# Kernel tuning notes

Hardware: AMD Instinct MI355X
Metric: run time of the kernel (lower is better)

Reference implementation:

```python
import jax, jax.numpy as jnp
import numpy as np

B, EEG_D, FMRI_D, BD, H, NC = 131072, 128, 64, 128, 4, 2
HD = BD // H  # head dim = 32
EPS = 1e-5

def layernorm(x, g, b):
    m = jnp.mean(x, axis=-1, keepdims=True)
    v = jnp.var(x, axis=-1, keepdims=True)
    return (x - m) * jax.lax.rsqrt(v + EPS) * g + b

def setup_inputs() -> dict:
    key = jax.random.key(0)
    ks = jax.random.split(key, 24)
    r = lambda i, shape, s=0.05: jax.random.normal(ks[i], shape, dtype=jnp.float32) * s
    return {
        'eeg_feats': jax.random.normal(ks[0], (B, EEG_D), dtype=jnp.float32),
        'fmri_feats': jax.random.normal(ks[1], (B, FMRI_D), dtype=jnp.float32),
        # projections (weights stored [in, out])
        'We': r(2, (EEG_D, BD)), 'be': jnp.zeros((BD,)),
        'ge': jnp.ones((BD,)), 'bge': jnp.zeros((BD,)),
        'Wf': r(3, (FMRI_D, BD)), 'bf': jnp.zeros((BD,)),
        'gf': jnp.ones((BD,)), 'bgf': jnp.zeros((BD,)),
        # multihead attention
        'Wq': r(4, (BD, BD)), 'bq': jnp.zeros((BD,)),
        'Wk': r(5, (BD, BD)), 'bk': jnp.zeros((BD,)),
        'Wv': r(6, (BD, BD)), 'bv': jnp.zeros((BD,)),
        'Wo': r(7, (BD, BD)), 'bo': jnp.zeros((BD,)),
        # learned fusion
        'fusion_logits': jnp.zeros((2,)),
        'temperature': jnp.ones(()),
        # classifier
        'Wc1': r(8, (BD, BD // 2)), 'bc1': jnp.zeros((BD // 2,)),
        'gc': jnp.ones((BD // 2,)), 'bgc': jnp.zeros((BD // 2,)),
        'Wc2': r(9, (BD // 2, NC)), 'bc2': jnp.zeros((NC,)),
    }

def reference(eeg_feats, fmri_feats, We, be, ge, bge, Wf, bf, gf, bgf,
              Wq, bq, Wk, bk, Wv, bv, Wo, bo, fusion_logits, temperature,
              Wc1, bc1, gc, bgc, Wc2, bc2):
    # modality projections: Linear + LN + GELU (dropout off at eval)
    eeg_p = jax.nn.gelu(layernorm(eeg_feats @ We + be, ge, bge), approximate=False)
    fmri_p = jax.nn.gelu(layernorm(fmri_feats @ Wf + bf, gf, bgf), approximate=False)

    # cross-attention: query = eeg_p (1 token), kv = [eeg_p, fmri_p] (2 tokens)
    seq = jnp.stack([eeg_p, fmri_p], axis=1)                 # [B, 2, BD]
    q = (eeg_p @ Wq + bq).reshape(B, H, HD)                  # [B, H, HD]
    k = (seq @ Wk + bk).reshape(B, 2, H, HD)
    v = (seq @ Wv + bv).reshape(B, 2, H, HD)
    scores = jnp.einsum('bhd,bkhd->bhk', q, k) / jnp.sqrt(jnp.float32(HD))
    attn = jax.nn.softmax(scores, axis=-1)                   # [B, H, 2]
    ctx = jnp.einsum('bhk,bkhd->bhd', attn, v).reshape(B, BD)
    eeg_enh = ctx @ Wo + bo                                  # [B, BD]

    # learned temperature-scaled fusion over [eeg_enhanced, fmri_proj]
    w = jax.nn.softmax(fusion_logits / temperature, axis=0)
    fused = w[0] * eeg_enh + w[1] * fmri_p                   # [B, BD]

    # classifier: Linear + LN + ReLU + Linear
    h = jax.nn.relu(layernorm(fused @ Wc1 + bc1, gc, bgc))
    logits = h @ Wc2 + bc2                                   # [B, NC]
    return logits
```

## Files before the change

kernel.cpp:

```cpp
#include <hip/hip_runtime.h>
#include <math.h>

#define EPS 1e-5f
#define SCALE 0.17677669529663687f

#define OFF_We  0
#define OFF_Wf  16384
#define OFF_Wq  24576
#define OFF_Wk  40960
#define OFF_Wv  57344
#define OFF_Wo  73728
#define OFF_Wc1 90112
#define PACK_TOTAL 98304

#define CHUNK 4096

#define BOFF(r, c) ((((r) << 7) + (c)) ^ (((r) & 7) << 3))

typedef __bf16 bf16x8 __attribute__((ext_vector_type(8)));
typedef float f32x4 __attribute__((ext_vector_type(4)));
typedef unsigned short ushort_t;
typedef unsigned short ushortx4 __attribute__((ext_vector_type(4)));

__device__ __forceinline__ ushort_t f2bf(float x) {
    return __builtin_bit_cast(ushort_t, (__bf16)x);
}
__device__ __forceinline__ float bf2f(ushort_t v) {
    unsigned u = ((unsigned)v) << 16;
    return __builtin_bit_cast(float, u);
}

__device__ __forceinline__ ushort_t f2bf_sw(float x) {
    unsigned u = __builtin_bit_cast(unsigned, x);
    u = (u + 0x7fffu + ((u >> 16) & 1u)) >> 16;
    return (ushort_t)u;
}

#define DPPADD(x, ctrl) \
    ((x) + __builtin_bit_cast(float, __builtin_amdgcn_update_dpp( \
        __builtin_bit_cast(int, (x)), __builtin_bit_cast(int, (x)), (ctrl), 0xF, 0xF, false)))

__device__ __forceinline__ float rowsum16(float x) {
    x = DPPADD(x, 0x121);
    x = DPPADD(x, 0x122);
    x = DPPADD(x, 0x124);
    x = DPPADD(x, 0x128);
    return x;
}

__device__ __forceinline__ float gelu_fast(float x) {
    float x2 = x * x;
    float t = fmaf(-0.10294313843f, x2, -2.30220842f);
#if __has_builtin(__builtin_amdgcn_exp2f)
    float e = __builtin_amdgcn_exp2f(x * t);
#else
    float e = __expf(x * t * 0.6931471806f);
#endif
    return x * __builtin_amdgcn_rcpf(1.0f + e);
}

__global__ __launch_bounds__(256) void pack_all(
    const float* __restrict__ We, const float* __restrict__ Wf,
    const float* __restrict__ Wq, const float* __restrict__ Wk,
    const float* __restrict__ Wv, const float* __restrict__ Wo,
    const float* __restrict__ Wc1, ushort_t* __restrict__ ws)
{
    int o = blockIdx.x * 256 + threadIdx.x;
    if (o >= PACK_TOTAL) return;
    const float* W; int K, N, base;
    if (o < OFF_Wf)        { W = We;  K = 128; N = 128; base = OFF_We; }
    else if (o < OFF_Wq)   { W = Wf;  K = 64;  N = 128; base = OFF_Wf; }
    else if (o < OFF_Wk)   { W = Wq;  K = 128; N = 128; base = OFF_Wq; }
    else if (o < OFF_Wv)   { W = Wk;  K = 128; N = 128; base = OFF_Wk; }
    else if (o < OFF_Wo)   { W = Wv;  K = 128; N = 128; base = OFF_Wv; }
    else if (o < OFF_Wc1)  { W = Wo;  K = 128; N = 128; base = OFF_Wo; }
    else                   { W = Wc1; K = 128; N = 64;  base = OFF_Wc1; }
    int e = o - base;
    int j = e & 7, l = (e >> 3) & 63, rest = e >> 9;
    int KS = K >> 5;
    int s = rest % KS, t = rest / KS;
    int k = s * 32 + ((l >> 4) << 3) + j;
    int n = (t << 4) + (l & 15);
    ws[o] = f2bf_sw(W[k * N + n]);
}

template<int KS>
__device__ __forceinline__ void load_af(bf16x8 af[KS], const ushort_t* A, int lane)
{
    const int quad = lane >> 4, l16 = lane & 15;
    #pragma unroll
    for (int ks = 0; ks < KS; ++ks)
        af[ks] = *(const bf16x8*)(A + BOFF(l16, ks * 32 + quad * 8));
}

template<int KS, int NT>
__device__ __forceinline__ void mma_c(const bf16x8 af[KS], const ushort_t* sW,
                                      f32x4* acc, int lane)
{
    #pragma unroll
    for (int t = 0; t < NT; ++t)
        #pragma unroll
        for (int ks = 0; ks < KS; ++ks) {
            bf16x8 bb = *(const bf16x8*)(sW + ((t * KS + ks) * 64 + lane) * 8);
            acc[t] = __builtin_amdgcn_mfma_f32_16x16x32_bf16(af[ks], bb, acc[t], 0, 0, 0);
        }
}

__global__ __launch_bounds__(256, 3) void fusion_stage(
    const float* __restrict__ eeg, const float* __restrict__ fmri,
    const float* __restrict__ be, const float* __restrict__ ge, const float* __restrict__ bge,
    const float* __restrict__ bfb, const float* __restrict__ gf, const float* __restrict__ bgf,
    const float* __restrict__ bq, const float* __restrict__ bk, const float* __restrict__ bv,
    const float* __restrict__ bo,
    const float* __restrict__ fusion_logits, const float* __restrict__ temperature,
    const float* __restrict__ bc1, const float* __restrict__ gc, const float* __restrict__ bgc,
    const float* __restrict__ Wc2, const float* __restrict__ bc2,
    const ushort_t* __restrict__ ws, float* __restrict__ out)
{
    __shared__ __align__(16) ushort_t sW[CHUNK];
    __shared__ __align__(16) ushort_t B1[4][16 * 128];
    __shared__ __align__(16) ushort_t B2[4][16 * 128];

    const int tid = threadIdx.x;
    const int wave = tid >> 6, lane = tid & 63;
    const int quad = lane >> 4, l16 = lane & 15;
    const int rowbase = blockIdx.x * 64 + wave * 16;
    ushort_t* b1 = B1[wave];
    ushort_t* b2 = B2[wave];

    auto stageW = [&](int offU) {
        __syncthreads();
        const char* g = (const char*)(ws + offU) + tid * 16;
        char* l = (char*)sW + tid * 16;
        __builtin_amdgcn_global_load_lds(
            (const __attribute__((address_space(1))) void*)g,
            (__attribute__((address_space(3))) void*)l, 16, 0, 0);
        __builtin_amdgcn_global_load_lds(
            (const __attribute__((address_space(1))) void*)(g + 4096),
            (__attribute__((address_space(3))) void*)(l + 4096), 16, 0, 0);
        __syncthreads();
    };

    {
        const float4* src = (const float4*)(eeg + (size_t)rowbase * 128);
        #pragma unroll
        for (int i = 0; i < 8; ++i) {
            int idx = i * 64 + lane;
            float4 v = src[idx];
            int r = idx >> 5, k4 = (idx & 31) * 4;
            *(ushortx4*)&b1[BOFF(r, k4)] =
                (ushortx4){f2bf(v.x), f2bf(v.y), f2bf(v.z), f2bf(v.w)};
        }
        const float4* srcf = (const float4*)(fmri + (size_t)rowbase * 64);
        #pragma unroll
        for (int i = 0; i < 4; ++i) {
            int idx = i * 64 + lane;
            float4 v = srcf[idx];
            int r = idx >> 4, k4 = (idx & 15) * 4;
            *(ushortx4*)&b2[BOFF(r, k4)] =
                (ushortx4){f2bf(v.x), f2bf(v.y), f2bf(v.z), f2bf(v.w)};
        }
    }

    float meanS[4], rstdS[4];

    {
        bf16x8 afR[4]; load_af<4>(afR, b1, lane);
        f32x4 acc[8];
        #pragma unroll
        for (int nt = 0; nt < 8; ++nt) {
            float b = be[nt * 16 + l16];
            acc[nt] = (f32x4){b, b, b, b};
        }
        #pragma unroll
        for (int c = 0; c < 4; ++c) {
            stageW(OFF_We + c * CHUNK);
            mma_c<4, 2>(afR, sW, acc + c * 2, lane);
        }
        #pragma unroll
        for (int r = 0; r < 4; ++r) {
            float s = 0.f, ss = 0.f;
            #pragma unroll
            for (int nt = 0; nt < 8; ++nt) { float x = acc[nt][r]; s += x; ss = fmaf(x, x, ss); }
            s = rowsum16(s); ss = rowsum16(ss);
            float m = s * (1.f / 128.f);
            meanS[r] = m;
            rstdS[r] = rsqrtf(ss * (1.f / 128.f) - m * m + EPS);
        }
        #pragma unroll
        for (int nt = 0; nt < 8; ++nt) {
            float g = ge[nt * 16 + l16], bb = bge[nt * 16 + l16];
            #pragma unroll
            for (int r = 0; r < 4; ++r) {
                float x = (acc[nt][r] - meanS[r]) * rstdS[r] * g + bb;
                b1[BOFF(quad * 4 + r, nt * 16 + l16)] = f2bf(gelu_fast(x));
            }
        }
    }

    f32x4 fpv[8];
    {
        bf16x8 afR[2]; load_af<2>(afR, b2, lane);
        f32x4 acc[8];
        #pragma unroll
        for (int nt = 0; nt < 8; ++nt) {
            float b = bfb[nt * 16 + l16];
            acc[nt] = (f32x4){b, b, b, b};
        }
        stageW(OFF_Wf);          mma_c<2, 4>(afR, sW, acc + 0, lane);
        stageW(OFF_Wf + CHUNK);  mma_c<2, 4>(afR, sW, acc + 4, lane);
        #pragma unroll
        for (int r = 0; r < 4; ++r) {
            float s = 0.f, ss = 0.f;
            #pragma unroll
            for (int nt = 0; nt < 8; ++nt) { float x = acc[nt][r]; s += x; ss = fmaf(x, x, ss); }
            s = rowsum16(s); ss = rowsum16(ss);
            float m = s * (1.f / 128.f);
            meanS[r] = m;
            rstdS[r] = rsqrtf(ss * (1.f / 128.f) - m * m + EPS);
        }
        #pragma unroll
        for (int nt = 0; nt < 8; ++nt) {
            float g = gf[nt * 16 + l16], bb = bgf[nt * 16 + l16];
            #pragma unroll
            for (int r = 0; r < 4; ++r) {
                float x = (acc[nt][r] - meanS[r]) * rstdS[r] * g + bb;
                float gv = gelu_fast(x);
                fpv[nt][r] = gv;
                b2[BOFF(quad * 4 + r, nt * 16 + l16)] = f2bf(gv);
            }
        }
    }

    bf16x8 afE[4]; load_af<4>(afE, b1, lane);
    bf16x8 afF[4]; load_af<4>(afF, b2, lane);

    f32x4 q[8];
    {
        #pragma unroll
        for (int nt = 0; nt < 8; ++nt) {
            float b = bq[nt * 16 + l16];
            q[nt] = (f32x4){b, b, b, b};
        }
        #pragma unroll
        for (int c = 0; c < 4; ++c) {
            stageW(OFF_Wq + c * CHUNK);
            mma_c<4, 2>(afE, sW, q + c * 2, lane);
        }
    }

    float a0v[4][4];
    {
        float pd[4][4];
        #pragma unroll
        for (int h = 0; h < 4; ++h)
            #pragma unroll
            for (int r = 0; r < 4; ++r) pd[h][r] = 0.f;
        #pragma unroll
        for (int c = 0; c < 4; ++c) {
            stageW(OFF_Wk + c * CHUNK);
            #pragma unroll
            for (int tl = 0; tl < 2; ++tl) {
                int nt = c * 2 + tl;
                f32x4 e = {0.f, 0.f, 0.f, 0.f}, f = {0.f, 0.f, 0.f, 0.f};
                #pragma unroll
                for (int ks = 0; ks < 4; ++ks) {
                    bf16x8 bb = *(const bf16x8*)(sW + ((tl * 4 + ks) * 64 + lane) * 8);
                    e = __builtin_amdgcn_mfma_f32_16x16x32_bf16(afE[ks], bb, e, 0, 0, 0);
                    f = __builtin_amdgcn_mfma_f32_16x16x32_bf16(afF[ks], bb, f, 0, 0, 0);
                }
                int h = nt >> 1;
                #pragma unroll
                for (int r = 0; r < 4; ++r)
                    pd[h][r] = fmaf(q[nt][r], e[r] - f[r], pd[h][r]);
            }
        }
        #pragma unroll
        for (int h = 0; h < 4; ++h)
            #pragma unroll
            for (int r = 0; r < 4; ++r) {
                float d = rowsum16(pd[h][r]) * SCALE;
                a0v[h][r] = __builtin_amdgcn_rcpf(1.0f + __expf(-d));
            }
    }

    #pragma unroll
    for (int c = 0; c < 4; ++c) {
        stageW(OFF_Wv + c * CHUNK);
        #pragma unroll
        for (int tl = 0; tl < 2; ++tl) {
            int nt = c * 2 + tl;
            float b = bv[nt * 16 + l16];
            f32x4 e = {b, b, b, b}, f = {b, b, b, b};
            #pragma unroll
            for (int ks = 0; ks < 4; ++ks) {
                bf16x8 bb = *(const bf16x8*)(sW + ((tl * 4 + ks) * 64 + lane) * 8);
                e = __builtin_amdgcn_mfma_f32_16x16x32_bf16(afE[ks], bb, e, 0, 0, 0);
                f = __builtin_amdgcn_mfma_f32_16x16x32_bf16(afF[ks], bb, f, 0, 0, 0);
            }
            int h = nt >> 1;
            #pragma unroll
            for (int r = 0; r < 4; ++r) {
                float c0 = fmaf(a0v[h][r], e[r] - f[r], f[r]);
                b1[BOFF(quad * 4 + r, nt * 16 + l16)] = f2bf(c0);
            }
        }
    }

    {
        bf16x8 afC[4]; load_af<4>(afC, b1, lane);
        f32x4 acc[8];
        #pragma unroll
        for (int nt = 0; nt < 8; ++nt) {
            float b = bo[nt * 16 + l16];
            acc[nt] = (f32x4){b, b, b, b};
        }
        #pragma unroll
        for (int c = 0; c < 4; ++c) {
            stageW(OFF_Wo + c * CHUNK);
            mma_c<4, 2>(afC, sW, acc + c * 2, lane);
        }
        float t = temperature[0];
        float dl = (fusion_logits[0] - fusion_logits[1]) / t;
        float w0 = __builtin_amdgcn_rcpf(1.0f + __expf(-dl));
        float w1 = 1.0f - w0;
        #pragma unroll
        for (int nt = 0; nt < 8; ++nt)
            #pragma unroll
            for (int r = 0; r < 4; ++r)
                b1[BOFF(quad * 4 + r, nt * 16 + l16)] = f2bf(w0 * acc[nt][r] + w1 * fpv[nt][r]);
    }

    {
        bf16x8 afU[4]; load_af<4>(afU, b1, lane);
        f32x4 accH[4];
        #pragma unroll
        for (int nt = 0; nt < 4; ++nt) {
            float b = bc1[nt * 16 + l16];
            accH[nt] = (f32x4){b, b, b, b};
        }
        stageW(OFF_Wc1);          mma_c<4, 2>(afU, sW, accH + 0, lane);
        stageW(OFF_Wc1 + CHUNK);  mma_c<4, 2>(afU, sW, accH + 2, lane);
        #pragma unroll
        for (int r = 0; r < 4; ++r) {
            float s = 0.f, ss = 0.f;
            #pragma unroll
            for (int nt = 0; nt < 4; ++nt) { float x = accH[nt][r]; s += x; ss = fmaf(x, x, ss); }
            s = rowsum16(s); ss = rowsum16(ss);
            float m = s * (1.f / 64.f);
            meanS[r] = m;
            rstdS[r] = rsqrtf(ss * (1.f / 64.f) - m * m + EPS);
        }
        float hv[4][4];
        #pragma unroll
        for (int nt = 0; nt < 4; ++nt) {
            float g = gc[nt * 16 + l16], bb = bgc[nt * 16 + l16];
            #pragma unroll
            for (int r = 0; r < 4; ++r) {
                float x = (accH[nt][r] - meanS[r]) * rstdS[r] * g + bb;
                hv[nt][r] = fmaxf(x, 0.0f);
            }
        }
        float w2v[4][2];
        #pragma unroll
        for (int nt = 0; nt < 4; ++nt) {
            float2 w = *(const float2*)&Wc2[(nt * 16 + l16) * 2];
            w2v[nt][0] = w.x; w2v[nt][1] = w.y;
        }
        float o0c = bc2[0], o1c = bc2[1];
        #pragma unroll
        for (int r = 0; r < 4; ++r) {
            float p0 = 0.f, p1 = 0.f;
            #pragma unroll
            for (int nt = 0; nt < 4; ++nt) {
                p0 = fmaf(hv[nt][r], w2v[nt][0], p0);
                p1 = fmaf(hv[nt][r], w2v[nt][1], p1);
            }
            p0 = rowsum16(p0); p1 = rowsum16(p1);
            if (l16 == 0) {
                int row = rowbase + quad * 4 + r;
                float2 o; o.x = p0 + o0c; o.y = p1 + o1c;
                *(float2*)&out[row * 2] = o;
            }
        }
    }
}

extern "C" void kernel_launch(void* const* d_in, const int* in_sizes, int n_in,
                              void* d_out, int out_size, void* d_ws, size_t ws_size,
                              hipStream_t stream) {
    const float* eeg  = (const float*)d_in[0];
    const float* fmri = (const float*)d_in[1];
    const float* We   = (const float*)d_in[2];
    const float* be   = (const float*)d_in[3];
    const float* ge   = (const float*)d_in[4];
    const float* bge  = (const float*)d_in[5];
    const float* Wf   = (const float*)d_in[6];
    const float* bf   = (const float*)d_in[7];
    const float* gf   = (const float*)d_in[8];
    const float* bgf  = (const float*)d_in[9];
    const float* Wq   = (const float*)d_in[10];
    const float* bq   = (const float*)d_in[11];
    const float* Wk   = (const float*)d_in[12];
    const float* bk   = (const float*)d_in[13];
    const float* Wv   = (const float*)d_in[14];
    const float* bv   = (const float*)d_in[15];
    const float* Wo   = (const float*)d_in[16];
    const float* bo   = (const float*)d_in[17];
    const float* fl   = (const float*)d_in[18];
    const float* temp = (const float*)d_in[19];
    const float* Wc1  = (const float*)d_in[20];
    const float* bc1  = (const float*)d_in[21];
    const float* gc   = (const float*)d_in[22];
    const float* bgc  = (const float*)d_in[23];
    const float* Wc2  = (const float*)d_in[24];
    const float* bc2  = (const float*)d_in[25];
    float* out = (float*)d_out;
    ushort_t* ws = (ushort_t*)d_ws;

    hipLaunchKernelGGL(pack_all, dim3((PACK_TOTAL + 255) / 256), dim3(256), 0, stream,
                       We, Wf, Wq, Wk, Wv, Wo, Wc1, ws);

    int B = in_sizes[0] / 128;
    int grid = B / 64;
    hipLaunchKernelGGL(fusion_stage, dim3(grid), dim3(256), 0, stream,
                       eeg, fmri, be, ge, bge, bf, gf, bgf,
                       bq, bk, bv, bo, fl, temp, bc1, gc, bgc, Wc2, bc2,
                       ws, out);
}
```

Baseline: 235.3 us.

## Double-buffer weight chunk staging and prefetch next chunk during MFMA compute

Weight staging changes from a single LDS buffer with two barriers per chunk to two ping-pong buffers. Each step issues an asynchronous global-to-LDS load of the next chunk right after one barrier, so weight fetches overlap the current chunk's MFMAs. The second per-wave activation buffer is removed and its data reuses the first buffer in sequence, which cuts LDS usage. The cost is more LDS for weights, and correctness now depends on the barrier waiting for the outstanding async loads.

```diff
diff --git a/kernel.cpp b/kernel.cpp
--- a/kernel.cpp
+++ b/kernel.cpp
@@ -14,6 +14,7 @@
 #define PACK_TOTAL 98304
 
 #define CHUNK 4096
+#define NCHUNK 24
 
 #define BOFF(r, c) ((((r) << 7) + (c)) ^ (((r) & 7) << 3))
 
@@ -94,14 +95,14 @@
 }
 
 template<int KS, int NT>
-__device__ __forceinline__ void mma_c(const bf16x8 af[KS], const ushort_t* sW,
+__device__ __forceinline__ void mma_c(const bf16x8 af[KS], const ushort_t* sWb,
                                       f32x4* acc, int lane)
 {
     #pragma unroll
     for (int t = 0; t < NT; ++t)
         #pragma unroll
         for (int ks = 0; ks < KS; ++ks) {
-            bf16x8 bb = *(const bf16x8*)(sW + ((t * KS + ks) * 64 + lane) * 8);
+            bf16x8 bb = *(const bf16x8*)(sWb + ((t * KS + ks) * 64 + lane) * 8);
             acc[t] = __builtin_amdgcn_mfma_f32_16x16x32_bf16(af[ks], bb, acc[t], 0, 0, 0);
         }
 }
@@ -117,29 +118,36 @@
     const float* __restrict__ Wc2, const float* __restrict__ bc2,
     const ushort_t* __restrict__ ws, float* __restrict__ out)
 {
-    __shared__ __align__(16) ushort_t sW[CHUNK];
+    __shared__ __align__(16) ushort_t sW[2][CHUNK];
     __shared__ __align__(16) ushort_t B1[4][16 * 128];
-    __shared__ __align__(16) ushort_t B2[4][16 * 128];
 
     const int tid = threadIdx.x;
     const int wave = tid >> 6, lane = tid & 63;
     const int quad = lane >> 4, l16 = lane & 15;
     const int rowbase = blockIdx.x * 64 + wave * 16;
     ushort_t* b1 = B1[wave];
-    ushort_t* b2 = B2[wave];
-
-    auto stageW = [&](int offU) {
-        __syncthreads();
-        const char* g = (const char*)(ws + offU) + tid * 16;
-        char* l = (char*)sW + tid * 16;
+
+    auto prefetch = [&](int c) {
+        const char* g = (const char*)(ws + c * CHUNK) + tid * 16;
+        char* l = (char*)(sW[c & 1]) + tid * 16;
         __builtin_amdgcn_global_load_lds(
             (const __attribute__((address_space(1))) void*)g,
             (__attribute__((address_space(3))) void*)l, 16, 0, 0);
         __builtin_amdgcn_global_load_lds(
             (const __attribute__((address_space(1))) void*)(g + 4096),
             (__attribute__((address_space(3))) void*)(l + 4096), 16, 0, 0);
+    };
+
+    int ck = 0;
+    auto step = [&]() -> const ushort_t* {
         __syncthreads();
+        if (ck + 1 < NCHUNK) prefetch(ck + 1);
+        const ushort_t* p = sW[ck & 1];
+        ++ck;
+        return p;
     };
+
+    prefetch(0);
 
     {
         const float4* src = (const float4*)(eeg + (size_t)rowbase * 128);
@@ -151,32 +159,35 @@
             *(ushortx4*)&b1[BOFF(r, k4)] =
                 (ushortx4){f2bf(v.x), f2bf(v.y), f2bf(v.z), f2bf(v.w)};
         }
+    }
+    bf16x8 afR[4]; load_af<4>(afR, b1, lane);
+
+    {
         const float4* srcf = (const float4*)(fmri + (size_t)rowbase * 64);
         #pragma unroll
         for (int i = 0; i < 4; ++i) {
             int idx = i * 64 + lane;
             float4 v = srcf[idx];
             int r = idx >> 4, k4 = (idx & 15) * 4;
-            *(ushortx4*)&b2[BOFF(r, k4)] =
+            *(ushortx4*)&b1[BOFF(r, k4)] =
                 (ushortx4){f2bf(v.x), f2bf(v.y), f2bf(v.z), f2bf(v.w)};
         }
     }
+    bf16x8 afRf[2]; load_af<2>(afRf, b1, lane);
 
     float meanS[4], rstdS[4];
 
     {
-        bf16x8 afR[4]; load_af<4>(afR, b1, lane);
         f32x4 acc[8];
         #pragma unroll
         for (int nt = 0; nt < 8; ++nt) {
             float b = be[nt * 16 + l16];
             acc[nt] = (f32x4){b, b, b, b};
         }
-        #pragma unroll
-        for (int c = 0; c < 4; ++c) {
-            stageW(OFF_We + c * CHUNK);
-            mma_c<4, 2>(afR, sW, acc + c * 2, lane);
-        }
+        mma_c<4, 2>(afR, step(), acc + 0, lane);
+        mma_c<4, 2>(afR, step(), acc + 2, lane);
+        mma_c<4, 2>(afR, step(), acc + 4, lane);
+        mma_c<4, 2>(afR, step(), acc + 6, lane);
         #pragma unroll
         for (int r = 0; r < 4; ++r) {
             float s = 0.f, ss = 0.f;
@@ -200,15 +211,14 @@
 
     f32x4 fpv[8];
     {
-        bf16x8 afR[2]; load_af<2>(afR, b2, lane);
         f32x4 acc[8];
         #pragma unroll
         for (int nt = 0; nt < 8; ++nt) {
             float b = bfb[nt * 16 + l16];
             acc[nt] = (f32x4){b, b, b, b};
         }
-        stageW(OFF_Wf);          mma_c<2, 4>(afR, sW, acc + 0, lane);
-        stageW(OFF_Wf + CHUNK);  mma_c<2, 4>(afR, sW, acc + 4, lane);
+        mma_c<2, 4>(afRf, step(), acc + 0, lane);
+        mma_c<2, 4>(afRf, step(), acc + 4, lane);
         #pragma unroll
         for (int r = 0; r < 4; ++r) {
             float s = 0.f, ss = 0.f;
@@ -225,15 +235,18 @@
             #pragma unroll
             for (int r = 0; r < 4; ++r) {
                 float x = (acc[nt][r] - meanS[r]) * rstdS[r] * g + bb;
-                float gv = gelu_fast(x);
-                fpv[nt][r] = gv;
-                b2[BOFF(quad * 4 + r, nt * 16 + l16)] = f2bf(gv);
+                fpv[nt][r] = gelu_fast(x);
             }
         }
     }
 
     bf16x8 afE[4]; load_af<4>(afE, b1, lane);
-    bf16x8 afF[4]; load_af<4>(afF, b2, lane);
+    #pragma unroll
+    for (int nt = 0; nt < 8; ++nt)
+        #pragma unroll
+        for (int r = 0; r < 4; ++r)
+            b1[BOFF(quad * 4 + r, nt * 16 + l16)] = f2bf(fpv[nt][r]);
+    bf16x8 afF[4]; load_af<4>(afF, b1, lane);
 
     f32x4 q[8];
     {
@@ -242,30 +255,29 @@
             float b = bq[nt * 16 + l16];
             q[nt] = (f32x4){b, b, b, b};
         }
+        mma_c<4, 2>(afE, step(), q + 0, lane);
+        mma_c<4, 2>(afE, step(), q + 2, lane);
+        mma_c<4, 2>(afE, step(), q + 4, lane);
+        mma_c<4, 2>(afE, step(), q + 6, lane);
+    }
+
+    float a0v[4][4];
+    {
+        float pd[4][4];
+        #pragma unroll
+        for (int h = 0; h < 4; ++h)
+            #pragma unroll
+            for (int r = 0; r < 4; ++r) pd[h][r] = 0.f;
         #pragma unroll
         for (int c = 0; c < 4; ++c) {
-            stageW(OFF_Wq + c * CHUNK);
-            mma_c<4, 2>(afE, sW, q + c * 2, lane);
-        }
-    }
-
-    float a0v[4][4];
-    {
-        float pd[4][4];
-        #pragma unroll
-        for (int h = 0; h < 4; ++h)
-            #pragma unroll
-            for (int r = 0; r < 4; ++r) pd[h][r] = 0.f;
-        #pragma unroll
-        for (int c = 0; c < 4; ++c) {
-            stageW(OFF_Wk + c * CHUNK);
+            const ushort_t* p = step();
             #pragma unroll
             for (int tl = 0; tl < 2; ++tl) {
                 int nt = c * 2 + tl;
                 f32x4 e = {0.f, 0.f, 0.f, 0.f}, f = {0.f, 0.f, 0.f, 0.f};
                 #pragma unroll
                 for (int ks = 0; ks < 4; ++ks) {
-                    bf16x8 bb = *(const bf16x8*)(sW + ((tl * 4 + ks) * 64 + lane) * 8);
+                    bf16x8 bb = *(const bf16x8*)(p + ((tl * 4 + ks) * 64 + lane) * 8);
                     e = __builtin_amdgcn_mfma_f32_16x16x32_bf16(afE[ks], bb, e, 0, 0, 0);
                     f = __builtin_amdgcn_mfma_f32_16x16x32_bf16(afF[ks], bb, f, 0, 0, 0);
                 }
@@ -286,7 +298,7 @@
 
     #pragma unroll
     for (int c = 0; c < 4; ++c) {
-        stageW(OFF_Wv + c * CHUNK);
+        const ushort_t* p = step();
         #pragma unroll
         for (int tl = 0; tl < 2; ++tl) {
             int nt = c * 2 + tl;
@@ -294,7 +306,7 @@
             f32x4 e = {b, b, b, b}, f = {b, b, b, b};
             #pragma unroll
             for (int ks = 0; ks < 4; ++ks) {
-                bf16x8 bb = *(const bf16x8*)(sW + ((tl * 4 + ks) * 64 + lane) * 8);
+                bf16x8 bb = *(const bf16x8*)(p + ((tl * 4 + ks) * 64 + lane) * 8);
                 e = __builtin_amdgcn_mfma_f32_16x16x32_bf16(afE[ks], bb, e, 0, 0, 0);
                 f = __builtin_amdgcn_mfma_f32_16x16x32_bf16(afF[ks], bb, f, 0, 0, 0);
             }
@@ -315,11 +327,10 @@
             float b = bo[nt * 16 + l16];
             acc[nt] = (f32x4){b, b, b, b};
         }
-        #pragma unroll
-        for (int c = 0; c < 4; ++c) {
-            stageW(OFF_Wo + c * CHUNK);
-            mma_c<4, 2>(afC, sW, acc + c * 2, lane);
-        }
+        mma_c<4, 2>(afC, step(), acc + 0, lane);
+        mma_c<4, 2>(afC, step(), acc + 2, lane);
+        mma_c<4, 2>(afC, step(), acc + 4, lane);
+        mma_c<4, 2>(afC, step(), acc + 6, lane);
         float t = temperature[0];
         float dl = (fusion_logits[0] - fusion_logits[1]) / t;
         float w0 = __builtin_amdgcn_rcpf(1.0f + __expf(-dl));
@@ -339,8 +350,8 @@
             float b = bc1[nt * 16 + l16];
             accH[nt] = (f32x4){b, b, b, b};
         }
-        stageW(OFF_Wc1);          mma_c<4, 2>(afU, sW, accH + 0, lane);
-        stageW(OFF_Wc1 + CHUNK);  mma_c<4, 2>(afU, sW, accH + 2, lane);
+        mma_c<4, 2>(afU, step(), accH + 0, lane);
+        mma_c<4, 2>(afU, step(), accH + 2, lane);
         #pragma unroll
         for (int r = 0; r < 4; ++r) {
             float s = 0.f, ss = 0.f;
```

After: 230.9 us. About the same (-1.9%).

## Stage weights in 32KB chunks to cut barrier count and drop second activation buffer

Applied to the files above, without the earlier changes.

Weight staging grows from 8KB to 32KB chunks, so the packed weights load in 6 stages instead of 24, each stage followed by __syncthreads. The matmuls are regrouped so each chunk covers the tail of one weight matrix and the head of the next, and the K/V projections are split across chunk boundaries. The separate B2 activation buffer is removed and B1 is reused, which reorders loads and stores. This cuts barrier and load-issue overhead, but the larger LDS footprint (about 48KB total) may reduce the number of blocks resident per CU and weaken latency hiding.

```diff
diff --git a/kernel.cpp b/kernel.cpp
--- a/kernel.cpp
+++ b/kernel.cpp
@@ -13,7 +13,8 @@
 #define OFF_Wc1 90112
 #define PACK_TOTAL 98304
 
-#define CHUNK 4096
+#define CHUNK 16384
+#define HALF  8192
 
 #define BOFF(r, c) ((((r) << 7) + (c)) ^ (((r) & 7) << 3))
 
@@ -94,14 +95,14 @@
 }
 
 template<int KS, int NT>
-__device__ __forceinline__ void mma_c(const bf16x8 af[KS], const ushort_t* sW,
+__device__ __forceinline__ void mma_c(const bf16x8 af[KS], const ushort_t* p,
                                       f32x4* acc, int lane)
 {
     #pragma unroll
     for (int t = 0; t < NT; ++t)
         #pragma unroll
         for (int ks = 0; ks < KS; ++ks) {
-            bf16x8 bb = *(const bf16x8*)(sW + ((t * KS + ks) * 64 + lane) * 8);
+            bf16x8 bb = *(const bf16x8*)(p + ((t * KS + ks) * 64 + lane) * 8);
             acc[t] = __builtin_amdgcn_mfma_f32_16x16x32_bf16(af[ks], bb, acc[t], 0, 0, 0);
         }
 }
@@ -119,25 +120,22 @@
 {
     __shared__ __align__(16) ushort_t sW[CHUNK];
     __shared__ __align__(16) ushort_t B1[4][16 * 128];
-    __shared__ __align__(16) ushort_t B2[4][16 * 128];
 
     const int tid = threadIdx.x;
     const int wave = tid >> 6, lane = tid & 63;
     const int quad = lane >> 4, l16 = lane & 15;
     const int rowbase = blockIdx.x * 64 + wave * 16;
     ushort_t* b1 = B1[wave];
-    ushort_t* b2 = B2[wave];
-
-    auto stageW = [&](int offU) {
+
+    auto stageW = [&](int c) {
         __syncthreads();
-        const char* g = (const char*)(ws + offU) + tid * 16;
+        const char* g = (const char*)(ws + c * CHUNK) + tid * 16;
         char* l = (char*)sW + tid * 16;
-        __builtin_amdgcn_global_load_lds(
-            (const __attribute__((address_space(1))) void*)g,
-            (__attribute__((address_space(3))) void*)l, 16, 0, 0);
-        __builtin_amdgcn_global_load_lds(
-            (const __attribute__((address_space(1))) void*)(g + 4096),
-            (__attribute__((address_space(3))) void*)(l + 4096), 16, 0, 0);
+        #pragma unroll
+        for (int i = 0; i < 8; ++i)
+            __builtin_amdgcn_global_load_lds(
+                (const __attribute__((address_space(1))) void*)(g + i * 4096),
+                (__attribute__((address_space(3))) void*)(l + i * 4096), 16, 0, 0);
         __syncthreads();
     };
 
@@ -151,32 +149,33 @@
             *(ushortx4*)&b1[BOFF(r, k4)] =
                 (ushortx4){f2bf(v.x), f2bf(v.y), f2bf(v.z), f2bf(v.w)};
         }
+    }
+    bf16x8 afR[4]; load_af<4>(afR, b1, lane);
+
+    {
         const float4* srcf = (const float4*)(fmri + (size_t)rowbase * 64);
         #pragma unroll
         for (int i = 0; i < 4; ++i) {
             int idx = i * 64 + lane;
             float4 v = srcf[idx];
             int r = idx >> 4, k4 = (idx & 15) * 4;
-            *(ushortx4*)&b2[BOFF(r, k4)] =
+            *(ushortx4*)&b1[BOFF(r, k4)] =
                 (ushortx4){f2bf(v.x), f2bf(v.y), f2bf(v.z), f2bf(v.w)};
         }
     }
+    bf16x8 afRf[2]; load_af<2>(afRf, b1, lane);
 
     float meanS[4], rstdS[4];
 
-    {
-        bf16x8 afR[4]; load_af<4>(afR, b1, lane);
+    stageW(0);
+    {
         f32x4 acc[8];
         #pragma unroll
         for (int nt = 0; nt < 8; ++nt) {
             float b = be[nt * 16 + l16];
             acc[nt] = (f32x4){b, b, b, b};
         }
-        #pragma unroll
-        for (int c = 0; c < 4; ++c) {
-            stageW(OFF_We + c * CHUNK);
-            mma_c<4, 2>(afR, sW, acc + c * 2, lane);
-        }
+        mma_c<4, 8>(afR, sW, acc, lane);
         #pragma unroll
         for (int r = 0; r < 4; ++r) {
             float s = 0.f, ss = 0.f;
@@ -199,16 +198,17 @@
     }
 
     f32x4 fpv[8];
-    {
-        bf16x8 afR[2]; load_af<2>(afR, b2, lane);
+    f32x4 q[8];
+    bf16x8 afE[4], afF[4];
+    stageW(1);
+    {
         f32x4 acc[8];
         #pragma unroll
         for (int nt = 0; nt < 8; ++nt) {
             float b = bfb[nt * 16 + l16];
             acc[nt] = (f32x4){b, b, b, b};
         }
-        stageW(OFF_Wf);          mma_c<2, 4>(afR, sW, acc + 0, lane);
-        stageW(OFF_Wf + CHUNK);  mma_c<2, 4>(afR, sW, acc + 4, lane);
+        mma_c<2, 8>(afRf, sW, acc, lane);
         #pragma unroll
         for (int r = 0; r < 4; ++r) {
             float s = 0.f, ss = 0.f;
@@ -225,73 +225,56 @@
             #pragma unroll
             for (int r = 0; r < 4; ++r) {
                 float x = (acc[nt][r] - meanS[r]) * rstdS[r] * g + bb;
-                float gv = gelu_fast(x);
-                fpv[nt][r] = gv;
-                b2[BOFF(quad * 4 + r, nt * 16 + l16)] = f2bf(gv);
-            }
-        }
-    }
-
-    bf16x8 afE[4]; load_af<4>(afE, b1, lane);
-    bf16x8 afF[4]; load_af<4>(afF, b2, lane);
-
-    f32x4 q[8];
-    {
+                fpv[nt][r] = gelu_fast(x);
+            }
+        }
+        load_af<4>(afE, b1, lane);
+        #pragma unroll
+        for (int nt = 0; nt < 8; ++nt)
+            #pragma unroll
+            for (int r = 0; r < 4; ++r)
+                b1[BOFF(quad * 4 + r, nt * 16 + l16)] = f2bf(fpv[nt][r]);
+        load_af<4>(afF, b1, lane);
         #pragma unroll
         for (int nt = 0; nt < 8; ++nt) {
             float b = bq[nt * 16 + l16];
             q[nt] = (f32x4){b, b, b, b};
         }
-        #pragma unroll
-        for (int c = 0; c < 4; ++c) {
-            stageW(OFF_Wq + c * CHUNK);
-            mma_c<4, 2>(afE, sW, q + c * 2, lane);
+        mma_c<4, 4>(afE, sW + HALF, q + 0, lane);
+    }
+
+    float pd[4][4];
+    #pragma unroll
+    for (int h = 0; h < 4; ++h)
+        #pragma unroll
+        for (int r = 0; r < 4; ++r) pd[h][r] = 0.f;
+    stageW(2);
+    {
+        mma_c<4, 4>(afE, sW, q + 4, lane);
+        #pragma unroll
+        for (int tl = 0; tl < 4; ++tl) {
+            int nt = tl;
+            f32x4 e = {0.f, 0.f, 0.f, 0.f}, f = {0.f, 0.f, 0.f, 0.f};
+            #pragma unroll
+            for (int ks = 0; ks < 4; ++ks) {
+                bf16x8 bb = *(const bf16x8*)(sW + HALF + ((tl * 4 + ks) * 64 + lane) * 8);
+                e = __builtin_amdgcn_mfma_f32_16x16x32_bf16(afE[ks], bb, e, 0, 0, 0);
+                f = __builtin_amdgcn_mfma_f32_16x16x32_bf16(afF[ks], bb, f, 0, 0, 0);
+            }
+            int h = nt >> 1;
+            #pragma unroll
+            for (int r = 0; r < 4; ++r)
+                pd[h][r] = fmaf(q[nt][r], e[r] - f[r], pd[h][r]);
         }
     }
 
     float a0v[4][4];
-    {
-        float pd[4][4];
-        #pragma unroll
-        for (int h = 0; h < 4; ++h)
-            #pragma unroll
-            for (int r = 0; r < 4; ++r) pd[h][r] = 0.f;
-        #pragma unroll
-        for (int c = 0; c < 4; ++c) {
-            stageW(OFF_Wk + c * CHUNK);
-            #pragma unroll
-            for (int tl = 0; tl < 2; ++tl) {
-                int nt = c * 2 + tl;
-                f32x4 e = {0.f, 0.f, 0.f, 0.f}, f = {0.f, 0.f, 0.f, 0.f};
-                #pragma unroll
-                for (int ks = 0; ks < 4; ++ks) {
-                    bf16x8 bb = *(const bf16x8*)(sW + ((tl * 4 + ks) * 64 + lane) * 8);
-                    e = __builtin_amdgcn_mfma_f32_16x16x32_bf16(afE[ks], bb, e, 0, 0, 0);
-                    f = __builtin_amdgcn_mfma_f32_16x16x32_bf16(afF[ks], bb, f, 0, 0, 0);
-                }
-                int h = nt >> 1;
-                #pragma unroll
-                for (int r = 0; r < 4; ++r)
-                    pd[h][r] = fmaf(q[nt][r], e[r] - f[r], pd[h][r]);
-            }
-        }
-        #pragma unroll
-        for (int h = 0; h < 4; ++h)
-            #pragma unroll
-            for (int r = 0; r < 4; ++r) {
-                float d = rowsum16(pd[h][r]) * SCALE;
-                a0v[h][r] = __builtin_amdgcn_rcpf(1.0f + __expf(-d));
-            }
-    }
-
-    #pragma unroll
-    for (int c = 0; c < 4; ++c) {
-        stageW(OFF_Wv + c * CHUNK);
-        #pragma unroll
-        for (int tl = 0; tl < 2; ++tl) {
-            int nt = c * 2 + tl;
-            float b = bv[nt * 16 + l16];
-            f32x4 e = {b, b, b, b}, f = {b, b, b, b};
+    stageW(3);
+    {
+        #pragma unroll
+        for (int tl = 0; tl < 4; ++tl) {
+            int nt = 4 + tl;
+            f32x4 e = {0.f, 0.f, 0.f, 0.f}, f = {0.f, 0.f, 0.f, 0.f};
             #pragma unroll
             for (int ks = 0; ks < 4; ++ks) {
                 bf16x8 bb = *(const bf16x8*)(sW + ((tl * 4 + ks) * 64 + lane) * 8);
@@ -300,6 +283,29 @@
             }
             int h = nt >> 1;
             #pragma unroll
+            for (int r = 0; r < 4; ++r)
+                pd[h][r] = fmaf(q[nt][r], e[r] - f[r], pd[h][r]);
+        }
+        #pragma unroll
+        for (int h = 0; h < 4; ++h)
+            #pragma unroll
+            for (int r = 0; r < 4; ++r) {
+                float d = rowsum16(pd[h][r]) * SCALE;
+                a0v[h][r] = __builtin_amdgcn_rcpf(1.0f + __expf(-d));
+            }
+        #pragma unroll
+        for (int tl = 0; tl < 4; ++tl) {
+            int nt = tl;
+            float b = bv[nt * 16 + l16];
+            f32x4 e = {b, b, b, b}, f = {b, b, b, b};
+            #pragma unroll
+            for (int ks = 0; ks < 4; ++ks) {
+                bf16x8 bb = *(const bf16x8*)(sW + HALF + ((tl * 4 + ks) * 64 + lane) * 8);
+                e = __builtin_amdgcn_mfma_f32_16x16x32_bf16(afE[ks], bb, e, 0, 0, 0);
+                f = __builtin_amdgcn_mfma_f32_16x16x32_bf16(afF[ks], bb, f, 0, 0, 0);
+            }
+            int h = nt >> 1;
+            #pragma unroll
             for (int r = 0; r < 4; ++r) {
                 float c0 = fmaf(a0v[h][r], e[r] - f[r], f[r]);
                 b1[BOFF(quad * 4 + r, nt * 16 + l16)] = f2bf(c0);
@@ -307,19 +313,40 @@
         }
     }
 
-    {
-        bf16x8 afC[4]; load_af<4>(afC, b1, lane);
-        f32x4 acc[8];
+    f32x4 acc6[8];
+    bf16x8 afC[4];
+    stageW(4);
+    {
+        #pragma unroll
+        for (int tl = 0; tl < 4; ++tl) {
+            int nt = 4 + tl;
+            float b = bv[nt * 16 + l16];
+            f32x4 e = {b, b, b, b}, f = {b, b, b, b};
+            #pragma unroll
+            for (int ks = 0; ks < 4; ++ks) {
+                bf16x8 bb = *(const bf16x8*)(sW + ((tl * 4 + ks) * 64 + lane) * 8);
+                e = __builtin_amdgcn_mfma_f32_16x16x32_bf16(afE[ks], bb, e, 0, 0, 0);
+                f = __builtin_amdgcn_mfma_f32_16x16x32_bf16(afF[ks], bb, f, 0, 0, 0);
+            }
+            int h = nt >> 1;
+            #pragma unroll
+            for (int r = 0; r < 4; ++r) {
+                float c0 = fmaf(a0v[h][r], e[r] - f[r], f[r]);
+                b1[BOFF(quad * 4 + r, nt * 16 + l16)] = f2bf(c0);
+            }
+        }
+        load_af<4>(afC, b1, lane);
         #pragma unroll
         for (int nt = 0; nt < 8; ++nt) {
             float b = bo[nt * 16 + l16];
-            acc[nt] = (f32x4){b, b, b, b};
-        }
-        #pragma unroll
-        for (int c = 0; c < 4; ++c) {
-            stageW(OFF_Wo + c * CHUNK);
-            mma_c<4, 2>(afC, sW, acc + c * 2, lane);
-        }
+            acc6[nt] = (f32x4){b, b, b, b};
+        }
+        mma_c<4, 4>(afC, sW + HALF, acc6 + 0, lane);
+    }
+
+    stageW(5);
+    {
+        mma_c<4, 4>(afC, sW, acc6 + 4, lane);
         float t = temperature[0];
         float dl = (fusion_logits[0] - fusion_logits[1]) / t;
         float w0 = __builtin_amdgcn_rcpf(1.0f + __expf(-dl));
@@ -328,10 +355,7 @@
         for (int nt = 0; nt < 8; ++nt)
             #pragma unroll
             for (int r = 0; r < 4; ++r)
-                b1[BOFF(quad * 4 + r, nt * 16 + l16)] = f2bf(w0 * acc[nt][r] + w1 * fpv[nt][r]);
-    }
-
-    {
+                b1[BOFF(quad * 4 + r, nt * 16 + l16)] = f2bf(w0 * acc6[nt][r] + w1 * fpv[nt][r]);
         bf16x8 afU[4]; load_af<4>(afU, b1, lane);
         f32x4 accH[4];
         #pragma unroll
@@ -339,8 +363,7 @@
             float b = bc1[nt * 16 + l16];
             accH[nt] = (f32x4){b, b, b, b};
         }
-        stageW(OFF_Wc1);          mma_c<4, 2>(afU, sW, accH + 0, lane);
-        stageW(OFF_Wc1 + CHUNK);  mma_c<4, 2>(afU, sW, accH + 2, lane);
+        mma_c<4, 4>(afU, sW + HALF, accH, lane);
         #pragma unroll
         for (int r = 0; r < 4; ++r) {
             float s = 0.f, ss = 0.f;
```

Result: faster. 228.2 us (-3.0%).
